# Kernel tuning notes

Hardware: AMD Instinct MI355X
Metric: run time of the kernel (lower is better)

The kernel has to match this reference:

```python
import jax, jax.numpy as jnp
import numpy as np

T, B = 256, 128
VOCAB, E, H, L = 73640, 320, 512, 5
G = 4 * H  # gate dim 2048


def setup_inputs() -> dict:
    key = jax.random.key(0)
    ks = jax.random.split(key, 12)
    stdv = 1.0 / np.sqrt(H)
    u = lambda k, shape: jax.random.uniform(k, shape, jnp.float32, -stdv, stdv)
    tokens = jax.random.randint(ks[0], (T, B), 0, VOCAB)
    embed = jax.random.normal(ks[1], (VOCAB, E), jnp.float32) * 0.1
    # layer 0 (input dim E), directions stacked on axis 0
    W_ih0 = u(ks[2], (2, G, E))
    W_hh0 = u(ks[3], (2, G, H))
    b_ih0 = u(ks[4], (2, G))
    b_hh0 = u(ks[5], (2, G))
    # layers 1..4 (input dim 2H = concat of both directions)
    W_ih = u(ks[6], (L - 1, 2, G, 2 * H))
    W_hh = u(ks[7], (L - 1, 2, G, H))
    b_ih = u(ks[8], (L - 1, 2, G))
    b_hh = u(ks[9], (L - 1, 2, G))
    return {"tokens": tokens, "embed": embed, "W_ih0": W_ih0, "W_hh0": W_hh0,
            "b_ih0": b_ih0, "b_hh0": b_hh0, "W_ih": W_ih, "W_hh": W_hh,
            "b_ih": b_ih, "b_hh": b_hh}


def _lstm_both_dirs(x, h, c, Wi, Wh, bi, bh):
    # x: [B, in]; h, c: [2, B, H]; Wi: [2, 4H, in]; Wh: [2, 4H, H]; bi, bh: [2, 4H]
    gates = (jnp.einsum('bi,dgi->dbg', x, Wi)
             + jnp.einsum('dbh,dgh->dbg', h, Wh)
             + (bi + bh)[:, None, :])
    i, f, g, o = jnp.split(gates, 4, axis=-1)  # PyTorch gate order i,f,g,o
    c_new = jax.nn.sigmoid(f) * c + jax.nn.sigmoid(i) * jnp.tanh(g)
    h_new = jax.nn.sigmoid(o) * jnp.tanh(c_new)
    return h_new, c_new


def reference(tokens, embed, W_ih0, W_hh0, b_ih0, b_hh0, W_ih, W_hh, b_ih, b_hh):
    emb = embed[tokens]  # [T, B, E]
    Bsz = tokens.shape[1]
    h0 = jnp.zeros((L, 2, Bsz, H), jnp.float32)
    c0 = jnp.zeros((L, 2, Bsz, H), jnp.float32)

    def step(carry, x_t):
        h, c = carry
        hl, cl = _lstm_both_dirs(x_t, h[0], c[0], W_ih0, W_hh0, b_ih0, b_hh0)
        hs, cs = [hl], [cl]
        inp = jnp.concatenate([hl[0], hl[1]], axis=-1)  # [B, 2H]
        for l in range(L - 1):
            hl, cl = _lstm_both_dirs(inp, h[l + 1], c[l + 1],
                                     W_ih[l], W_hh[l], b_ih[l], b_hh[l])
            hs.append(hl); cs.append(cl)
            inp = jnp.concatenate([hl[0], hl[1]], axis=-1)
        return (jnp.stack(hs), jnp.stack(cs)), hs[-1]  # emit last-layer h [2, B, H]

    _, last_layer_h = jax.lax.scan(step, (h0, c0), emb)  # [T, 2, B, H]
    # LASEREmbedderI: take last layer, max-pool over the two directions
    return jnp.max(last_layer_h, axis=1)  # [T, B, H]
```

## Files before the change

kernel.cpp:

```cpp
#include <hip/hip_runtime.h>
#include <stdint.h>

typedef unsigned short u16;
typedef unsigned int   u32;
typedef unsigned long long u64;
typedef short bf16x8 __attribute__((ext_vector_type(8)));
typedef float f32x4  __attribute__((ext_vector_type(4)));

static_assert(sizeof(bf16x8) == 16, "bf16x8 must be 16B");

#define LOG2E 1.4426950408889634f
#define TCH 32
#define NSLOT 131072
#define HDIR  65536

__device__ __forceinline__ float bf2f(u16 u) { return __builtin_bit_cast(float, ((u32)u) << 16); }
__device__ __forceinline__ u16 f2bf(float f) {
  u32 x = __builtin_bit_cast(u32, f);
  return (u16)((x + 0x7fffu + ((x >> 16) & 1u)) >> 16);
}
__device__ __forceinline__ float sigm(float x) {
  return __builtin_amdgcn_rcpf(1.f + __builtin_amdgcn_exp2f(-LOG2E * x));
}
__device__ __forceinline__ float tanh_(float x) {
  return 1.f - 2.f * __builtin_amdgcn_rcpf(1.f + __builtin_amdgcn_exp2f(2.f * LOG2E * x));
}
__device__ __forceinline__ bf16x8 cvt8(const float* p) {
  bf16x8 r;
  #pragma unroll
  for (int j = 0; j < 8; ++j) r[j] = (short)f2bf(p[j]);
  return r;
}

__global__ void k_bias(const float* __restrict__ bi0, const float* __restrict__ bh0,
                       const float* __restrict__ bi, const float* __restrict__ bh,
                       float* __restrict__ out) {
  int i = blockIdx.x * blockDim.x + threadIdx.x;
  if (i < 4096) out[i] = bi0[i] + bh0[i];
  else if (i < 20480) out[i] = bi[i - 4096] + bh[i - 4096];
}

__device__ __forceinline__ void gemm_tile(
    u16* smem, const u16* hb, const float* emb, const int* tok,
    const float* Wif, const float* bias, u16* gx, int K, int t0,
    int d, int nt0, int tt)
{
  u16* As = smem;
  u16* Bs = smem + 8192;
  int* s_tok = (int*)(smem + 16384);
  int tid = threadIdx.x, lane = tid & 63, w = tid >> 6;
  int wm = w & 1, wn = w >> 1;
  int t = t0 + tt;
  if (tok && tid < 128) s_tok[tid] = tok[t * 128 + tid];
  __syncthreads();

  const float* Bbase = Wif + ((size_t)d * 2048 + nt0 * 128) * K;
  f32x4 acc[4][4];
  #pragma unroll
  for (int a = 0; a < 4; ++a)
    #pragma unroll
    for (int b = 0; b < 4; ++b) acc[a][b] = f32x4{0.f, 0.f, 0.f, 0.f};

  int nkt = K >> 6;
  for (int kt = 0; kt < nkt; ++kt) {
    #pragma unroll
    for (int i = 0; i < 4; ++i) {
      int s = tid + i * 256;
      int row = s >> 3, c = s & 7;
      int cs = c ^ (row & 7);
      bf16x8 va;
      if (tok) {
        va = cvt8(emb + (size_t)s_tok[row] * 320 + kt * 64 + c * 8);
      } else {
        int k = kt * 64 + c * 8;
        va = *(const bf16x8*)(hb + (size_t)(t + 1) * NSLOT + (size_t)(k >> 9) * HDIR
                              + (size_t)row * 512 + (k & 511));
      }
      bf16x8 vb = cvt8(Bbase + (size_t)row * K + kt * 64 + c * 8);
      *(bf16x8*)(&As[(row * 8 + cs) * 8]) = va;
      *(bf16x8*)(&Bs[(row * 8 + cs) * 8]) = vb;
    }
    __syncthreads();
    #pragma unroll
    for (int kk2 = 0; kk2 < 2; ++kk2) {
      int cl = kk2 * 4 + (lane >> 4);
      bf16x8 af[4], bfr[4];
      #pragma unroll
      for (int mt = 0; mt < 4; ++mt) {
        int row = wm * 64 + mt * 16 + (lane & 15);
        af[mt] = *(const bf16x8*)(&As[(row * 8 + (cl ^ (row & 7))) * 8]);
      }
      #pragma unroll
      for (int nt = 0; nt < 4; ++nt) {
        int row = wn * 64 + nt * 16 + (lane & 15);
        bfr[nt] = *(const bf16x8*)(&Bs[(row * 8 + (cl ^ (row & 7))) * 8]);
      }
      #pragma unroll
      for (int mt = 0; mt < 4; ++mt)
        #pragma unroll
        for (int nt = 0; nt < 4; ++nt)
          acc[mt][nt] = __builtin_amdgcn_mfma_f32_16x16x32_bf16(af[mt], bfr[nt], acc[mt][nt], 0, 0, 0);
    }
    __syncthreads();
  }
  #pragma unroll
  for (int nt = 0; nt < 4; ++nt) {
    int g = nt0 * 128 + wn * 64 + nt * 16 + (lane & 15);
    float bv = bias[d * 2048 + g];
    int q = g >> 9, hbb = (g >> 4) & 31, u = g & 15;
    size_t cb = (((size_t)d * 32 + hbb) * TCH + tt) * 8192;
    #pragma unroll
    for (int mt = 0; mt < 4; ++mt)
      #pragma unroll
      for (int r = 0; r < 4; ++r) {
        int b = wm * 64 + mt * 16 + (lane >> 4) * 4 + r;
        int ws2 = b >> 5, mts = (b >> 4) & 1, l4s = (b >> 2) & 3, rs = b & 3;
        gx[cb + (size_t)(ws2 * 64 + l4s * 16 + u) * 32 + mts * 16 + q * 4 + rs]
          = f2bf(acc[mt][nt][r] + bv);
      }
  }
}

__global__ __launch_bounds__(256) void k_gemm0(
    const float* __restrict__ emb, const int* __restrict__ tok,
    const float* __restrict__ Wif, const float* __restrict__ bias, u16* __restrict__ gx)
{
  __shared__ __align__(16) u16 smem[16640];
  int xt = blockIdx.x;
  gemm_tile(smem, nullptr, emb, tok, Wif, bias, gx, 320, 0, xt >> 4, xt & 15, blockIdx.y);
}

__device__ __forceinline__ void waitflags(const u32* fl, int lane, int w, u32 target) {
  const u32* p = fl + ((lane & 31) << 4) + w;
  u32 v;
  for (;;) {
    asm volatile("global_load_dword %0, %1, off sc0 sc1\n\ts_waitcnt vmcnt(0)"
                 : "=v"(v) : "v"(p) : "memory");
    if (__all((int)(v >= target))) break;
    __builtin_amdgcn_s_sleep(1);
  }
}

__global__ __launch_bounds__(256, 2) void k_fused(
    const float* __restrict__ Whf, const u16* __restrict__ gx_s,
    u16* __restrict__ hb, float* __restrict__ cbuf,
    u32* flags, u32 base, int t0, int hz,
    const float* __restrict__ emb, const int* __restrict__ tok_g,
    const float* __restrict__ Wif_g, const float* __restrict__ bias_g,
    u16* __restrict__ gx_g, int Kg, int t0g)
{
  __shared__ __align__(16) u16 smem[32768];
  int tid = threadIdx.x, lane = tid & 63, w = tid >> 6;

  if (blockIdx.x >= 64) {
    if (t0g < 0) return;
    #pragma unroll 1
    for (int i = 0; i < 4; ++i) {
      int tau = (blockIdx.x - 64) + i * 256;
      int xt = tau & 31, tt = tau >> 5;
      gemm_tile(smem, hb, emb, tok_g, Wif_g, bias_g, gx_g, Kg, t0g, xt >> 4, xt & 15, tt);
      __syncthreads();
    }
    return;
  }

  int d = blockIdx.x >> 5, hb_i = blockIdx.x & 31;
  const u32* fl = flags + d * 512;
  u32* myflag = flags + d * 512 + hb_i * 16 + w;
  u16* WhL = smem;
  for (int i = tid; i < 64 * 512; i += 256) {
    int r = i >> 9, k = i & 511;
    int grow = (r >> 4) * 512 + hb_i * 16 + (r & 15);
    WhL[(r << 9) + (k ^ ((r & 7) << 3))] = f2bf(Whf[((size_t)d * 2048 + grow) * 512 + k]);
  }

  int bb = w * 32;
  int l15 = lane & 15, l4 = lane >> 4;
  float c2[2][4];
  if (t0 == 0) {
    #pragma unroll
    for (int mt = 0; mt < 2; ++mt)
      #pragma unroll
      for (int r = 0; r < 4; ++r) c2[mt][r] = 0.f;
  } else {
    #pragma unroll
    for (int mt = 0; mt < 2; ++mt)
      #pragma unroll
      for (int r = 0; r < 4; ++r) {
        int b = bb + mt * 16 + l4 * 4 + r;
        c2[mt][r] = cbuf[((size_t)d * 128 + b) * 512 + hb_i * 16 + l15];
      }
  }
  if (hz) {
    for (int i = tid; i < 512; i += 256) {
      int b = i >> 2, j = i & 3;
      u64* p = (u64*)(hb + (size_t)d * HDIR + (size_t)b * 512 + hb_i * 16) + j;
      __hip_atomic_store(p, 0ull, __ATOMIC_RELAXED, __HIP_MEMORY_SCOPE_AGENT);
    }
  }
  __syncthreads();
  if (hz && lane == 0) {
    u32 iv = base + 1;
    asm volatile("global_store_dword %0, %1, off sc0 sc1" :: "v"(myflag), "v"(iv) : "memory");
  }
  int init1 = hz ? 1 : 0;
  __builtin_amdgcn_s_setprio(1);

  const u16* gxblk = gx_s + ((size_t)d * 32 + hb_i) * TCH * 8192 + (size_t)tid * 32;
  bf16x8 gxv4[4], gxn4[4];
  #pragma unroll
  for (int j = 0; j < 4; ++j) gxv4[j] = *(const bf16x8*)(gxblk + j * 8);
  #pragma unroll
  for (int j = 0; j < 4; ++j) gxn4[j] = *(const bf16x8*)(gxblk + 8192 + j * 8);

  for (int tt = 0; tt < TCH; ++tt) {
    int t = t0 + tt;
    u32 target = base + (u32)tt + (u32)init1;
    if (!(tt == 0 && !init1)) waitflags(fl, lane, w, target);

    const u16* hp = hb + (size_t)t * NSLOT + (size_t)d * HDIR;
    const u16* hpA = hp + (size_t)(bb + l15) * 512 + l4 * 8;
    const u16* hpB = hp + (size_t)(bb + 16 + l15) * 512 + l4 * 8;
    f32x4 h0[16], h1[16];
    asm volatile(
      "global_load_dwordx4 %0, %8, off sc0 sc1\n\t"
      "global_load_dwordx4 %1, %8, off offset:64 sc0 sc1\n\t"
      "global_load_dwordx4 %2, %8, off offset:128 sc0 sc1\n\t"
      "global_load_dwordx4 %3, %8, off offset:192 sc0 sc1\n\t"
      "global_load_dwordx4 %4, %8, off offset:256 sc0 sc1\n\t"
      "global_load_dwordx4 %5, %8, off offset:320 sc0 sc1\n\t"
      "global_load_dwordx4 %6, %8, off offset:384 sc0 sc1\n\t"
      "global_load_dwordx4 %7, %8, off offset:448 sc0 sc1"
      : "=&v"(h0[0]), "=&v"(h0[1]), "=&v"(h0[2]), "=&v"(h0[3]),
        "=&v"(h0[4]), "=&v"(h0[5]), "=&v"(h0[6]), "=&v"(h0[7])
      : "v"(hpA) : "memory");
    asm volatile(
      "global_load_dwordx4 %0, %8, off offset:512 sc0 sc1\n\t"
      "global_load_dwordx4 %1, %8, off offset:576 sc0 sc1\n\t"
      "global_load_dwordx4 %2, %8, off offset:640 sc0 sc1\n\t"
      "global_load_dwordx4 %3, %8, off offset:704 sc0 sc1\n\t"
      "global_load_dwordx4 %4, %8, off offset:768 sc0 sc1\n\t"
      "global_load_dwordx4 %5, %8, off offset:832 sc0 sc1\n\t"
      "global_load_dwordx4 %6, %8, off offset:896 sc0 sc1\n\t"
      "global_load_dwordx4 %7, %8, off offset:960 sc0 sc1"
      : "=&v"(h0[8]), "=&v"(h0[9]), "=&v"(h0[10]), "=&v"(h0[11]),
        "=&v"(h0[12]), "=&v"(h0[13]), "=&v"(h0[14]), "=&v"(h0[15])
      : "v"(hpA) : "memory");
    asm volatile(
      "global_load_dwordx4 %0, %8, off sc0 sc1\n\t"
      "global_load_dwordx4 %1, %8, off offset:64 sc0 sc1\n\t"
      "global_load_dwordx4 %2, %8, off offset:128 sc0 sc1\n\t"
      "global_load_dwordx4 %3, %8, off offset:192 sc0 sc1\n\t"
      "global_load_dwordx4 %4, %8, off offset:256 sc0 sc1\n\t"
      "global_load_dwordx4 %5, %8, off offset:320 sc0 sc1\n\t"
      "global_load_dwordx4 %6, %8, off offset:384 sc0 sc1\n\t"
      "global_load_dwordx4 %7, %8, off offset:448 sc0 sc1"
      : "=&v"(h1[0]), "=&v"(h1[1]), "=&v"(h1[2]), "=&v"(h1[3]),
        "=&v"(h1[4]), "=&v"(h1[5]), "=&v"(h1[6]), "=&v"(h1[7])
      : "v"(hpB) : "memory");
    asm volatile(
      "global_load_dwordx4 %0, %8, off offset:512 sc0 sc1\n\t"
      "global_load_dwordx4 %1, %8, off offset:576 sc0 sc1\n\t"
      "global_load_dwordx4 %2, %8, off offset:640 sc0 sc1\n\t"
      "global_load_dwordx4 %3, %8, off offset:704 sc0 sc1\n\t"
      "global_load_dwordx4 %4, %8, off offset:768 sc0 sc1\n\t"
      "global_load_dwordx4 %5, %8, off offset:832 sc0 sc1\n\t"
      "global_load_dwordx4 %6, %8, off offset:896 sc0 sc1\n\t"
      "global_load_dwordx4 %7, %8, off offset:960 sc0 sc1\n\t"
      "s_waitcnt vmcnt(0)"
      : "=&v"(h1[8]), "=&v"(h1[9]), "=&v"(h1[10]), "=&v"(h1[11]),
        "=&v"(h1[12]), "=&v"(h1[13]), "=&v"(h1[14]), "=&v"(h1[15])
      : "v"(hpB) : "memory");
    __builtin_amdgcn_sched_barrier(0);

    f32x4 acc[2][4];
    #pragma unroll
    for (int mt = 0; mt < 2; ++mt)
      #pragma unroll
      for (int q = 0; q < 4; ++q) acc[mt][q] = f32x4{0.f, 0.f, 0.f, 0.f};
    #pragma unroll
    for (int kk = 0; kk < 16; ++kk) {
      int kbase = kk * 32 + l4 * 8;
      bf16x8 a0 = __builtin_bit_cast(bf16x8, h0[kk]);
      bf16x8 a1 = __builtin_bit_cast(bf16x8, h1[kk]);
      #pragma unroll
      for (int q = 0; q < 4; ++q) {
        int r = q * 16 + l15;
        bf16x8 bv = *(const bf16x8*)(&WhL[(r << 9) + (kbase ^ ((r & 7) << 3))]);
        acc[0][q] = __builtin_amdgcn_mfma_f32_16x16x32_bf16(a0, bv, acc[0][q], 0, 0, 0);
        acc[1][q] = __builtin_amdgcn_mfma_f32_16x16x32_bf16(a1, bv, acc[1][q], 0, 0, 0);
      }
    }
    u16* ho = hb + (size_t)(t + 1) * NSLOT + (size_t)d * HDIR;
    u32 hvv[2][4];
    #pragma unroll
    for (int mt = 0; mt < 2; ++mt)
      #pragma unroll
      for (int r = 0; r < 4; ++r) {
        float gi = acc[mt][0][r] + bf2f((u16)gxv4[mt * 2][r]);
        float gf = acc[mt][1][r] + bf2f((u16)gxv4[mt * 2][4 + r]);
        float gg = acc[mt][2][r] + bf2f((u16)gxv4[mt * 2 + 1][r]);
        float go = acc[mt][3][r] + bf2f((u16)gxv4[mt * 2 + 1][4 + r]);
        float cn = sigm(gf) * c2[mt][r] + sigm(gi) * tanh_(gg);
        float hn = sigm(go) * tanh_(cn);
        c2[mt][r] = cn;
        hvv[mt][r] = (u32)f2bf(hn);
      }
    {
      u16* st0 = ho + (size_t)(bb + l4 * 4) * 512 + hb_i * 16 + l15;
      u16* st1 = st0 + 16 * 512;
      int tt2 = (tt + 2 < TCH) ? (tt + 2) : (TCH - 1);
      const u16* gaddr = gxblk + (size_t)tt2 * 8192;
      u32 fv = target + 1;
      f32x4 g0, g1, g2, g3;
      asm volatile(
        "global_store_short %13, %4, off sc0 sc1\n\t"
        "global_store_short %13, %5, off offset:1024 sc0 sc1\n\t"
        "global_store_short %13, %6, off offset:2048 sc0 sc1\n\t"
        "global_store_short %13, %7, off offset:3072 sc0 sc1\n\t"
        "global_store_short %14, %8, off sc0 sc1\n\t"
        "global_store_short %14, %9, off offset:1024 sc0 sc1\n\t"
        "global_store_short %14, %10, off offset:2048 sc0 sc1\n\t"
        "global_store_short %14, %11, off offset:3072 sc0 sc1\n\t"
        "global_load_dwordx4 %0, %15, off\n\t"
        "global_load_dwordx4 %1, %15, off offset:16\n\t"
        "global_load_dwordx4 %2, %15, off offset:32\n\t"
        "global_load_dwordx4 %3, %15, off offset:48\n\t"
        "s_waitcnt vmcnt(4)\n\t"
        "global_store_dword %16, %12, off sc0 sc1"
        : "=&v"(g0), "=&v"(g1), "=&v"(g2), "=&v"(g3)
        : "v"(hvv[0][0]), "v"(hvv[0][1]), "v"(hvv[0][2]), "v"(hvv[0][3]),
          "v"(hvv[1][0]), "v"(hvv[1][1]), "v"(hvv[1][2]), "v"(hvv[1][3]),
          "v"(fv), "v"(st0), "v"(st1), "v"(gaddr), "v"(myflag)
        : "memory");
      #pragma unroll
      for (int j = 0; j < 4; ++j) gxv4[j] = gxn4[j];
      gxn4[0] = __builtin_bit_cast(bf16x8, g0);
      gxn4[1] = __builtin_bit_cast(bf16x8, g1);
      gxn4[2] = __builtin_bit_cast(bf16x8, g2);
      gxn4[3] = __builtin_bit_cast(bf16x8, g3);
    }
  }
  #pragma unroll
  for (int mt = 0; mt < 2; ++mt)
    #pragma unroll
    for (int r = 0; r < 4; ++r) {
      int b = bb + mt * 16 + l4 * 4 + r;
      cbuf[((size_t)d * 128 + b) * 512 + hb_i * 16 + l15] = c2[mt][r];
    }
}

__global__ void k_final(const u16* __restrict__ hb, float* __restrict__ out, int n) {
  int i = blockIdx.x * 256 + threadIdx.x;
  if (i >= n) return;
  int t = i >> 16, rem = i & 65535;
  int b = rem >> 9, j = rem & 511;
  const u16* s = hb + (size_t)(t + 1) * NSLOT + (size_t)b * 512 + j;
  float a = bf2f(s[0]);
  float bv = bf2f(s[HDIR]);
  out[i] = fmaxf(a, bv);
}

extern "C" void kernel_launch(void* const* d_in, const int* in_sizes, int n_in,
                              void* d_out, int out_size, void* d_ws, size_t ws_size,
                              hipStream_t stream) {
  (void)in_sizes; (void)n_in; (void)out_size; (void)ws_size;
  const int*   tokens = (const int*)d_in[0];
  const float* embedW = (const float*)d_in[1];
  const float* W_ih0  = (const float*)d_in[2];
  const float* W_hh0  = (const float*)d_in[3];
  const float* b_ih0  = (const float*)d_in[4];
  const float* b_hh0  = (const float*)d_in[5];
  const float* W_ih   = (const float*)d_in[6];
  const float* W_hh   = (const float*)d_in[7];
  const float* b_ih   = (const float*)d_in[8];
  const float* b_hh   = (const float*)d_in[9];

  char* ws = (char*)d_ws;
  size_t off = 0;
  auto alloc = [&](size_t bytes) { void* p = ws + off; off += (bytes + 255) & ~(size_t)255; return p; };
  float* biasC = (float*)alloc(20480ull * 4);
  u16*   hbuf  = (u16*)alloc((size_t)257 * NSLOT * 2);
  u16*   gxA   = (u16*)alloc(16777216ull * 2);
  u16*   gxB   = (u16*)alloc(16777216ull * 2);
  float* cbuf  = (float*)alloc(131072ull * 4);
  u32*   flags = (u32*)alloc(8192);

  hipMemsetAsync(flags, 0, 8192, stream);
  k_bias<<<80, 256, 0, stream>>>(b_ih0, b_hh0, b_ih, b_hh, biasC);
  k_gemm0<<<dim3(32, 32), 256, 0, stream>>>(embedW, tokens, W_ih0, biasC, gxA);

  u32 base = 0;
  for (int l = 0; l < 5; ++l) {
    const float* Whf_l = l ? (W_hh + (size_t)(l - 1) * 2097152) : W_hh0;
    for (int c = 0; c < 8; ++c) {
      int g = l * 8 + c;
      u16* gx_s = (g & 1) ? gxB : gxA;
      u16* gx_g = (g & 1) ? gxA : gxB;
      int lg = (c < 7) ? l : l + 1;
      int cg = (c < 7) ? c + 1 : 0;
      int has_g = (lg <= 4);
      const float* Wif_g = (lg == 0) ? W_ih0 : (W_ih + (size_t)(lg - 1) * 4194304);
      const int* tok_g = (lg == 0) ? tokens : nullptr;
      int Kg = (lg == 0) ? 320 : 1024;
      k_fused<<<320, 256, 0, stream>>>(
          Whf_l, gx_s, hbuf, cbuf, flags, base, c * TCH, (l == 0 && c == 0) ? 1 : 0,
          embedW, tok_g, Wif_g, biasC + (size_t)lg * 4096, gx_g, Kg,
          has_g ? cg * TCH : -1);
      base += 40;
    }
  }
  k_final<<<65536, 256, 0, stream>>>(hbuf, (float*)d_out, 16777216);
}
```

Measured before the change: 10.25 ms.

## Run LSTM layers as a diagonal wavefront over time chunks

Replaces the layer-by-layer sequence of 40 fused launches with 36 wavefront launches. Each launch runs the recurrent scan for every (layer, chunk) cell on the current anti-diagonal, plus the input-projection GEMMs for the next diagonal, and the chunk size drops from 32 to 8 steps. GEMM tiles wait on flags from the layer below rather than on launch order. Hidden-state storage becomes a 16-slot ring per layer. The final direction max-pool moves into the last layer through atomicMax on order-preserving encoded floats, followed by a decode pass. The goal is to overlap the serial recurrence of different layers and use more CUs at once, at the cost of more cross-block spin-waiting, atomics on the output, and shorter chunks with more per-launch setup.

```diff
diff --git a/kernel.cpp b/kernel.cpp
--- a/kernel.cpp
+++ b/kernel.cpp
@@ -10,9 +10,10 @@
 static_assert(sizeof(bf16x8) == 16, "bf16x8 must be 16B");
 
 #define LOG2E 1.4426950408889634f
-#define TCH 32
+#define TCH 8
 #define NSLOT 131072
 #define HDIR  65536
+#define GXCELL 4194304ull
 
 __device__ __forceinline__ float bf2f(u16 u) { return __builtin_bit_cast(float, ((u32)u) << 16); }
 __device__ __forceinline__ u16 f2bf(float f) {
@@ -30,6 +31,10 @@
   #pragma unroll
   for (int j = 0; j < 8; ++j) r[j] = (short)f2bf(p[j]);
   return r;
+}
+__device__ __forceinline__ u32 encf(float f) {
+  u32 b = __builtin_bit_cast(u32, f);
+  return (b & 0x80000000u) ? ~b : (b | 0x80000000u);
 }
 
 __global__ void k_bias(const float* __restrict__ bi0, const float* __restrict__ bh0,
@@ -41,20 +46,21 @@
 }
 
 __device__ __forceinline__ void gemm_tile(
-    u16* smem, const u16* hb, const float* emb, const int* tok,
-    const float* Wif, const float* bias, u16* gx, int K, int t0,
-    int d, int nt0, int tt)
+    u16* smem, const u16* hbPrev, const float* emb, const int* tok,
+    const float* Wif, const float* bias, u16* gx, int K,
+    int c, int tt, int d, int nt0)
 {
   u16* As = smem;
   u16* Bs = smem + 8192;
   int* s_tok = (int*)(smem + 16384);
   int tid = threadIdx.x, lane = tid & 63, w = tid >> 6;
   int wm = w & 1, wn = w >> 1;
-  int t = t0 + tt;
+  int t = c * TCH + tt;
   if (tok && tid < 128) s_tok[tid] = tok[t * 128 + tid];
   __syncthreads();
 
   const float* Bbase = Wif + ((size_t)d * 2048 + nt0 * 128) * K;
+  int slot = (t + 1) & 15;
   f32x4 acc[4][4];
   #pragma unroll
   for (int a = 0; a < 4; ++a)
@@ -66,17 +72,17 @@
     #pragma unroll
     for (int i = 0; i < 4; ++i) {
       int s = tid + i * 256;
-      int row = s >> 3, c = s & 7;
-      int cs = c ^ (row & 7);
+      int row = s >> 3, cc = s & 7;
+      int cs = cc ^ (row & 7);
       bf16x8 va;
       if (tok) {
-        va = cvt8(emb + (size_t)s_tok[row] * 320 + kt * 64 + c * 8);
+        va = cvt8(emb + (size_t)s_tok[row] * 320 + kt * 64 + cc * 8);
       } else {
-        int k = kt * 64 + c * 8;
-        va = *(const bf16x8*)(hb + (size_t)(t + 1) * NSLOT + (size_t)(k >> 9) * HDIR
+        int k = kt * 64 + cc * 8;
+        va = *(const bf16x8*)(hbPrev + (size_t)slot * NSLOT + (size_t)(k >> 9) * HDIR
                               + (size_t)row * 512 + (k & 511));
       }
-      bf16x8 vb = cvt8(Bbase + (size_t)row * K + kt * 64 + c * 8);
+      bf16x8 vb = cvt8(Bbase + (size_t)row * K + kt * 64 + cc * 8);
       *(bf16x8*)(&As[(row * 8 + cs) * 8]) = va;
       *(bf16x8*)(&Bs[(row * 8 + cs) * 8]) = vb;
     }
@@ -127,46 +133,137 @@
 {
   __shared__ __align__(16) u16 smem[16640];
   int xt = blockIdx.x;
-  gemm_tile(smem, nullptr, emb, tok, Wif, bias, gx, 320, 0, xt >> 4, xt & 15, blockIdx.y);
+  gemm_tile(smem, nullptr, emb, tok, Wif, bias, gx, 320, 0, blockIdx.y, xt >> 4, xt & 15);
 }
 
 __device__ __forceinline__ void waitflags(const u32* fl, int lane, int w, u32 target) {
   const u32* p = fl + ((lane & 31) << 4) + w;
-  u32 v;
   for (;;) {
+    u32 v;
     asm volatile("global_load_dword %0, %1, off sc0 sc1\n\ts_waitcnt vmcnt(0)"
                  : "=v"(v) : "v"(p) : "memory");
     if (__all((int)(v >= target))) break;
     __builtin_amdgcn_s_sleep(1);
   }
 }
-
-__global__ __launch_bounds__(256, 2) void k_fused(
-    const float* __restrict__ Whf, const u16* __restrict__ gx_s,
-    u16* __restrict__ hb, float* __restrict__ cbuf,
-    u32* flags, u32 base, int t0, int hz,
-    const float* __restrict__ emb, const int* __restrict__ tok_g,
-    const float* __restrict__ Wif_g, const float* __restrict__ bias_g,
-    u16* __restrict__ gx_g, int Kg, int t0g)
+__device__ __forceinline__ void wait_all(const u32* flp, int lane, u32 target) {
+  const u32* p = flp + lane * 16;
+  for (;;) {
+    f32x4 v4;
+    asm volatile("global_load_dwordx4 %0, %1, off sc0 sc1\n\ts_waitcnt vmcnt(0)"
+                 : "=v"(v4) : "v"(p) : "memory");
+    u32 m0 = __builtin_bit_cast(u32, v4[0]), m1 = __builtin_bit_cast(u32, v4[1]);
+    u32 m2 = __builtin_bit_cast(u32, v4[2]), m3 = __builtin_bit_cast(u32, v4[3]);
+    u32 mn = m0 < m1 ? m0 : m1; mn = mn < m2 ? mn : m2; mn = mn < m3 ? mn : m3;
+    if (__all((int)(mn >= target))) break;
+    __builtin_amdgcn_s_sleep(2);
+  }
+}
+
+#define HB8A(P, D) \
+    asm volatile( \
+      "global_load_dwordx4 %0, %8, off sc0 sc1\n\t" \
+      "global_load_dwordx4 %1, %8, off offset:64 sc0 sc1\n\t" \
+      "global_load_dwordx4 %2, %8, off offset:128 sc0 sc1\n\t" \
+      "global_load_dwordx4 %3, %8, off offset:192 sc0 sc1\n\t" \
+      "global_load_dwordx4 %4, %8, off offset:256 sc0 sc1\n\t" \
+      "global_load_dwordx4 %5, %8, off offset:320 sc0 sc1\n\t" \
+      "global_load_dwordx4 %6, %8, off offset:384 sc0 sc1\n\t" \
+      "global_load_dwordx4 %7, %8, off offset:448 sc0 sc1" \
+      : "=&v"(D[0]), "=&v"(D[1]), "=&v"(D[2]), "=&v"(D[3]), \
+        "=&v"(D[4]), "=&v"(D[5]), "=&v"(D[6]), "=&v"(D[7]) \
+      : "v"(P) : "memory")
+#define HB8B(P, D) \
+    asm volatile( \
+      "global_load_dwordx4 %0, %8, off offset:512 sc0 sc1\n\t" \
+      "global_load_dwordx4 %1, %8, off offset:576 sc0 sc1\n\t" \
+      "global_load_dwordx4 %2, %8, off offset:640 sc0 sc1\n\t" \
+      "global_load_dwordx4 %3, %8, off offset:704 sc0 sc1\n\t" \
+      "global_load_dwordx4 %4, %8, off offset:768 sc0 sc1\n\t" \
+      "global_load_dwordx4 %5, %8, off offset:832 sc0 sc1\n\t" \
+      "global_load_dwordx4 %6, %8, off offset:896 sc0 sc1\n\t" \
+      "global_load_dwordx4 %7, %8, off offset:960 sc0 sc1" \
+      : "=&v"(D[8]), "=&v"(D[9]), "=&v"(D[10]), "=&v"(D[11]), \
+        "=&v"(D[12]), "=&v"(D[13]), "=&v"(D[14]), "=&v"(D[15]) \
+      : "v"(P) : "memory")
+
+#define STPF_BODY(FLAGOPS) \
+      asm volatile( \
+        "global_store_short %13, %4, off sc0 sc1\n\t" \
+        "global_store_short %13, %5, off offset:1024 sc0 sc1\n\t" \
+        "global_store_short %13, %6, off offset:2048 sc0 sc1\n\t" \
+        "global_store_short %13, %7, off offset:3072 sc0 sc1\n\t" \
+        "global_store_short %14, %8, off sc0 sc1\n\t" \
+        "global_store_short %14, %9, off offset:1024 sc0 sc1\n\t" \
+        "global_store_short %14, %10, off offset:2048 sc0 sc1\n\t" \
+        "global_store_short %14, %11, off offset:3072 sc0 sc1\n\t" \
+        "global_load_dwordx4 %0, %15, off\n\t" \
+        "global_load_dwordx4 %1, %15, off offset:16\n\t" \
+        "global_load_dwordx4 %2, %15, off offset:32\n\t" \
+        "global_load_dwordx4 %3, %15, off offset:48\n\t" \
+        "s_waitcnt vmcnt(4)\n\t" \
+        FLAGOPS \
+        : "=&v"(g0), "=&v"(g1), "=&v"(g2), "=&v"(g3) \
+        : "v"(hvv[0][0]), "v"(hvv[0][1]), "v"(hvv[0][2]), "v"(hvv[0][3]), \
+          "v"(hvv[1][0]), "v"(hvv[1][1]), "v"(hvv[1][2]), "v"(hvv[1][3]), \
+          "v"(fv), "v"(st0), "v"(st1), "v"(gaddr), "v"(myflag) \
+        : "memory")
+
+__global__ __launch_bounds__(256, 2) void k_wave(
+    int g,
+    const float* __restrict__ W_hh0, const float* __restrict__ W_hh,
+    const float* __restrict__ W_ih0, const float* __restrict__ W_ih,
+    const float* __restrict__ biasC, const float* __restrict__ emb,
+    const int* __restrict__ tok,
+    u16* __restrict__ hbuf, u16* __restrict__ gxb, float* __restrict__ cbuf,
+    u32* __restrict__ outU, u32* __restrict__ flags)
 {
   __shared__ __align__(16) u16 smem[32768];
   int tid = threadIdx.x, lane = tid & 63, w = tid >> 6;
-
-  if (blockIdx.x >= 64) {
-    if (t0g < 0) return;
+  int bx = blockIdx.x;
+  int llo_s = (g - 31 > 0) ? (g - 31) : 0;
+  int lhi_s = (g < 4) ? g : 4;
+  int nscan = lhi_s - llo_s + 1;
+
+  if (bx >= 64 * nscan) {
+    int D = g + 1;
+    if (D > 35) return;
+    int llo = (D - 31 > 0) ? (D - 31) : 0;
+    int lhi = (D < 4) ? D : 4;
+    int ncell = lhi - llo + 1;
+    int J = ncell * 256;
+    int gid = bx - 64 * nscan, NG = 512 - 64 * nscan;
     #pragma unroll 1
-    for (int i = 0; i < 4; ++i) {
-      int tau = (blockIdx.x - 64) + i * 256;
-      int xt = tau & 31, tt = tau >> 5;
-      gemm_tile(smem, hb, emb, tok_g, Wif_g, bias_g, gx_g, Kg, t0g, xt >> 4, xt & 15, tt);
+    for (int j = gid; j < J; j += NG) {
+      int tt = j / (ncell * 32);
+      int rem = j - tt * (ncell * 32);
+      int ci = rem >> 5, dnt = rem & 31;
+      int lg = llo + ci, cg = D - lg;
+      const float* Wif = lg ? (W_ih + (size_t)(lg - 1) * 4194304) : W_ih0;
+      int K = lg ? 1024 : 320;
+      const int* tokp = lg ? nullptr : tok;
+      const u16* hbPrev = lg ? (hbuf + (size_t)(lg - 1) * 16 * NSLOT) : nullptr;
+      u16* gxd = gxb + ((size_t)(lg * 2 + (cg & 1))) * GXCELL;
+      if (lg > 0 && w == 0)
+        wait_all(flags + (size_t)(lg - 1) * 1024, lane, 40u * cg + 2u + (u32)tt);
+      gemm_tile(smem, hbPrev, emb, tokp, Wif, biasC + (size_t)lg * 4096,
+                gxd, K, cg, tt, dnt >> 4, dnt & 15);
       __syncthreads();
     }
     return;
   }
 
-  int d = blockIdx.x >> 5, hb_i = blockIdx.x & 31;
-  const u32* fl = flags + d * 512;
-  u32* myflag = flags + d * 512 + hb_i * 16 + w;
+  int ci = bx >> 6, within = bx & 63;
+  int l = llo_s + ci, c = g - l;
+  int d = within >> 5, hb_i = within & 31;
+  const float* Whf = l ? (W_hh + (size_t)(l - 1) * 2097152) : W_hh0;
+  u16* hbL = hbuf + (size_t)l * 16 * NSLOT;
+  float* cbL = cbuf + (size_t)l * 131072;
+  const u16* gxs = gxb + ((size_t)(l * 2 + (c & 1))) * GXCELL;
+  u32* fl = flags + (size_t)l * 1024 + d * 512;
+  u32* myflag = fl + hb_i * 16 + w;
+  u32 base = 40u * (u32)c;
+
   u16* WhL = smem;
   for (int i = tid; i < 64 * 512; i += 256) {
     int r = i >> 9, k = i & 511;
@@ -177,100 +274,53 @@
   int bb = w * 32;
   int l15 = lane & 15, l4 = lane >> 4;
   float c2[2][4];
-  if (t0 == 0) {
+  if (c == 0) {
     #pragma unroll
     for (int mt = 0; mt < 2; ++mt)
       #pragma unroll
       for (int r = 0; r < 4; ++r) c2[mt][r] = 0.f;
+    for (int i = tid; i < 512; i += 256) {
+      int b = i >> 2, j = i & 3;
+      u64* p = (u64*)(hbL + (size_t)d * HDIR + (size_t)b * 512 + hb_i * 16) + j;
+      __hip_atomic_store(p, 0ull, __ATOMIC_RELAXED, __HIP_MEMORY_SCOPE_AGENT);
+    }
+    __syncthreads();
+    if (lane == 0) {
+      u32 iv = base + 1;
+      asm volatile("global_store_dword %0, %1, off sc0 sc1" :: "v"(myflag), "v"(iv) : "memory");
+    }
+    waitflags(fl, lane, w, base + 1);
   } else {
     #pragma unroll
     for (int mt = 0; mt < 2; ++mt)
       #pragma unroll
       for (int r = 0; r < 4; ++r) {
         int b = bb + mt * 16 + l4 * 4 + r;
-        c2[mt][r] = cbuf[((size_t)d * 128 + b) * 512 + hb_i * 16 + l15];
-      }
-  }
-  if (hz) {
-    for (int i = tid; i < 512; i += 256) {
-      int b = i >> 2, j = i & 3;
-      u64* p = (u64*)(hb + (size_t)d * HDIR + (size_t)b * 512 + hb_i * 16) + j;
-      __hip_atomic_store(p, 0ull, __ATOMIC_RELAXED, __HIP_MEMORY_SCOPE_AGENT);
-    }
-  }
-  __syncthreads();
-  if (hz && lane == 0) {
-    u32 iv = base + 1;
-    asm volatile("global_store_dword %0, %1, off sc0 sc1" :: "v"(myflag), "v"(iv) : "memory");
-  }
-  int init1 = hz ? 1 : 0;
+        c2[mt][r] = cbL[((size_t)d * 128 + b) * 512 + hb_i * 16 + l15];
+      }
+    __syncthreads();
+  }
   __builtin_amdgcn_s_setprio(1);
 
-  const u16* gxblk = gx_s + ((size_t)d * 32 + hb_i) * TCH * 8192 + (size_t)tid * 32;
+  const u16* gxblk = gxs + ((size_t)(d * 32 + hb_i) * TCH) * 8192 + (size_t)tid * 32;
   bf16x8 gxv4[4], gxn4[4];
   #pragma unroll
   for (int j = 0; j < 4; ++j) gxv4[j] = *(const bf16x8*)(gxblk + j * 8);
   #pragma unroll
   for (int j = 0; j < 4; ++j) gxn4[j] = *(const bf16x8*)(gxblk + 8192 + j * 8);
 
+  #pragma unroll 1
   for (int tt = 0; tt < TCH; ++tt) {
-    int t = t0 + tt;
-    u32 target = base + (u32)tt + (u32)init1;
-    if (!(tt == 0 && !init1)) waitflags(fl, lane, w, target);
-
-    const u16* hp = hb + (size_t)t * NSLOT + (size_t)d * HDIR;
+    int t = c * TCH + tt;
+    if (tt > 0) waitflags(fl, lane, w, base + 1 + (u32)tt);
+
+    const u16* hp = hbL + (size_t)(t & 15) * NSLOT + (size_t)d * HDIR;
     const u16* hpA = hp + (size_t)(bb + l15) * 512 + l4 * 8;
     const u16* hpB = hp + (size_t)(bb + 16 + l15) * 512 + l4 * 8;
     f32x4 h0[16], h1[16];
-    asm volatile(
-      "global_load_dwordx4 %0, %8, off sc0 sc1\n\t"
-      "global_load_dwordx4 %1, %8, off offset:64 sc0 sc1\n\t"
-      "global_load_dwordx4 %2, %8, off offset:128 sc0 sc1\n\t"
-      "global_load_dwordx4 %3, %8, off offset:192 sc0 sc1\n\t"
-      "global_load_dwordx4 %4, %8, off offset:256 sc0 sc1\n\t"
-      "global_load_dwordx4 %5, %8, off offset:320 sc0 sc1\n\t"
-      "global_load_dwordx4 %6, %8, off offset:384 sc0 sc1\n\t"
-      "global_load_dwordx4 %7, %8, off offset:448 sc0 sc1"
-      : "=&v"(h0[0]), "=&v"(h0[1]), "=&v"(h0[2]), "=&v"(h0[3]),
-        "=&v"(h0[4]), "=&v"(h0[5]), "=&v"(h0[6]), "=&v"(h0[7])
-      : "v"(hpA) : "memory");
-    asm volatile(
-      "global_load_dwordx4 %0, %8, off offset:512 sc0 sc1\n\t"
-      "global_load_dwordx4 %1, %8, off offset:576 sc0 sc1\n\t"
-      "global_load_dwordx4 %2, %8, off offset:640 sc0 sc1\n\t"
-      "global_load_dwordx4 %3, %8, off offset:704 sc0 sc1\n\t"
-      "global_load_dwordx4 %4, %8, off offset:768 sc0 sc1\n\t"
-      "global_load_dwordx4 %5, %8, off offset:832 sc0 sc1\n\t"
-      "global_load_dwordx4 %6, %8, off offset:896 sc0 sc1\n\t"
-      "global_load_dwordx4 %7, %8, off offset:960 sc0 sc1"
-      : "=&v"(h0[8]), "=&v"(h0[9]), "=&v"(h0[10]), "=&v"(h0[11]),
-        "=&v"(h0[12]), "=&v"(h0[13]), "=&v"(h0[14]), "=&v"(h0[15])
-      : "v"(hpA) : "memory");
-    asm volatile(
-      "global_load_dwordx4 %0, %8, off sc0 sc1\n\t"
-      "global_load_dwordx4 %1, %8, off offset:64 sc0 sc1\n\t"
-      "global_load_dwordx4 %2, %8, off offset:128 sc0 sc1\n\t"
-      "global_load_dwordx4 %3, %8, off offset:192 sc0 sc1\n\t"
-      "global_load_dwordx4 %4, %8, off offset:256 sc0 sc1\n\t"
-      "global_load_dwordx4 %5, %8, off offset:320 sc0 sc1\n\t"
-      "global_load_dwordx4 %6, %8, off offset:384 sc0 sc1\n\t"
-      "global_load_dwordx4 %7, %8, off offset:448 sc0 sc1"
-      : "=&v"(h1[0]), "=&v"(h1[1]), "=&v"(h1[2]), "=&v"(h1[3]),
-        "=&v"(h1[4]), "=&v"(h1[5]), "=&v"(h1[6]), "=&v"(h1[7])
-      : "v"(hpB) : "memory");
-    asm volatile(
-      "global_load_dwordx4 %0, %8, off offset:512 sc0 sc1\n\t"
-      "global_load_dwordx4 %1, %8, off offset:576 sc0 sc1\n\t"
-      "global_load_dwordx4 %2, %8, off offset:640 sc0 sc1\n\t"
-      "global_load_dwordx4 %3, %8, off offset:704 sc0 sc1\n\t"
-      "global_load_dwordx4 %4, %8, off offset:768 sc0 sc1\n\t"
-      "global_load_dwordx4 %5, %8, off offset:832 sc0 sc1\n\t"
-      "global_load_dwordx4 %6, %8, off offset:896 sc0 sc1\n\t"
-      "global_load_dwordx4 %7, %8, off offset:960 sc0 sc1\n\t"
-      "s_waitcnt vmcnt(0)"
-      : "=&v"(h1[8]), "=&v"(h1[9]), "=&v"(h1[10]), "=&v"(h1[11]),
-        "=&v"(h1[12]), "=&v"(h1[13]), "=&v"(h1[14]), "=&v"(h1[15])
-      : "v"(hpB) : "memory");
+    HB8A(hpA, h0); HB8B(hpA, h0);
+    HB8A(hpB, h1); HB8B(hpB, h1);
+    asm volatile("s_waitcnt vmcnt(0)" ::: "memory");
     __builtin_amdgcn_sched_barrier(0);
 
     f32x4 acc[2][4];
@@ -291,8 +341,9 @@
         acc[1][q] = __builtin_amdgcn_mfma_f32_16x16x32_bf16(a1, bv, acc[1][q], 0, 0, 0);
       }
     }
-    u16* ho = hb + (size_t)(t + 1) * NSLOT + (size_t)d * HDIR;
+    u16* ho = hbL + (size_t)((t + 1) & 15) * NSLOT + (size_t)d * HDIR;
     u32 hvv[2][4];
+    float hnf[2][4];
     #pragma unroll
     for (int mt = 0; mt < 2; ++mt)
       #pragma unroll
@@ -304,6 +355,7 @@
         float cn = sigm(gf) * c2[mt][r] + sigm(gi) * tanh_(gg);
         float hn = sigm(go) * tanh_(cn);
         c2[mt][r] = cn;
+        hnf[mt][r] = hn;
         hvv[mt][r] = (u32)f2bf(hn);
       }
     {
@@ -311,28 +363,19 @@
       u16* st1 = st0 + 16 * 512;
       int tt2 = (tt + 2 < TCH) ? (tt + 2) : (TCH - 1);
       const u16* gaddr = gxblk + (size_t)tt2 * 8192;
-      u32 fv = target + 1;
+      u32 fv = base + 2 + (u32)tt;
       f32x4 g0, g1, g2, g3;
-      asm volatile(
-        "global_store_short %13, %4, off sc0 sc1\n\t"
-        "global_store_short %13, %5, off offset:1024 sc0 sc1\n\t"
-        "global_store_short %13, %6, off offset:2048 sc0 sc1\n\t"
-        "global_store_short %13, %7, off offset:3072 sc0 sc1\n\t"
-        "global_store_short %14, %8, off sc0 sc1\n\t"
-        "global_store_short %14, %9, off offset:1024 sc0 sc1\n\t"
-        "global_store_short %14, %10, off offset:2048 sc0 sc1\n\t"
-        "global_store_short %14, %11, off offset:3072 sc0 sc1\n\t"
-        "global_load_dwordx4 %0, %15, off\n\t"
-        "global_load_dwordx4 %1, %15, off offset:16\n\t"
-        "global_load_dwordx4 %2, %15, off offset:32\n\t"
-        "global_load_dwordx4 %3, %15, off offset:48\n\t"
-        "s_waitcnt vmcnt(4)\n\t"
-        "global_store_dword %16, %12, off sc0 sc1"
-        : "=&v"(g0), "=&v"(g1), "=&v"(g2), "=&v"(g3)
-        : "v"(hvv[0][0]), "v"(hvv[0][1]), "v"(hvv[0][2]), "v"(hvv[0][3]),
-          "v"(hvv[1][0]), "v"(hvv[1][1]), "v"(hvv[1][2]), "v"(hvv[1][3]),
-          "v"(fv), "v"(st0), "v"(st1), "v"(gaddr), "v"(myflag)
-        : "memory");
+      if (lane == 0) { STPF_BODY("global_store_dword %16, %12, off sc0 sc1"); }
+      else          { STPF_BODY("s_nop 0"); }
+      if (l == 4) {
+        #pragma unroll
+        for (int mt = 0; mt < 2; ++mt)
+          #pragma unroll
+          for (int r = 0; r < 4; ++r) {
+            int b = bb + mt * 16 + l4 * 4 + r;
+            atomicMax(&outU[((size_t)t * 128 + b) * 512 + hb_i * 16 + l15], encf(hnf[mt][r]));
+          }
+      }
       #pragma unroll
       for (int j = 0; j < 4; ++j) gxv4[j] = gxn4[j];
       gxn4[0] = __builtin_bit_cast(bf16x8, g0);
@@ -346,19 +389,16 @@
     #pragma unroll
     for (int r = 0; r < 4; ++r) {
       int b = bb + mt * 16 + l4 * 4 + r;
-      cbuf[((size_t)d * 128 + b) * 512 + hb_i * 16 + l15] = c2[mt][r];
-    }
-}
-
-__global__ void k_final(const u16* __restrict__ hb, float* __restrict__ out, int n) {
+      cbL[((size_t)d * 128 + b) * 512 + hb_i * 16 + l15] = c2[mt][r];
+    }
+}
+
+__global__ void k_decode(u32* __restrict__ p, int n) {
   int i = blockIdx.x * 256 + threadIdx.x;
   if (i >= n) return;
-  int t = i >> 16, rem = i & 65535;
-  int b = rem >> 9, j = rem & 511;
-  const u16* s = hb + (size_t)(t + 1) * NSLOT + (size_t)b * 512 + j;
-  float a = bf2f(s[0]);
-  float bv = bf2f(s[HDIR]);
-  out[i] = fmaxf(a, bv);
+  u32 u = p[i];
+  u32 b = (u & 0x80000000u) ? (u ^ 0x80000000u) : ~u;
+  p[i] = b;
 }
 
 extern "C" void kernel_launch(void* const* d_in, const int* in_sizes, int n_in,
@@ -380,35 +420,20 @@
   size_t off = 0;
   auto alloc = [&](size_t bytes) { void* p = ws + off; off += (bytes + 255) & ~(size_t)255; return p; };
   float* biasC = (float*)alloc(20480ull * 4);
-  u16*   hbuf  = (u16*)alloc((size_t)257 * NSLOT * 2);
-  u16*   gxA   = (u16*)alloc(16777216ull * 2);
-  u16*   gxB   = (u16*)alloc(16777216ull * 2);
-  float* cbuf  = (float*)alloc(131072ull * 4);
-  u32*   flags = (u32*)alloc(8192);
-
-  hipMemsetAsync(flags, 0, 8192, stream);
+  u16*   hbuf  = (u16*)alloc((size_t)5 * 16 * NSLOT * 2);
+  u16*   gxb   = (u16*)alloc((size_t)10 * GXCELL * 2);
+  float* cbuf  = (float*)alloc((size_t)5 * 131072 * 4);
+  u32*   flags = (u32*)alloc(32768);
+
+  hipMemsetAsync(flags, 0, 32768, stream);
+  hipMemsetAsync(d_out, 0, (size_t)16777216 * 4, stream);
   k_bias<<<80, 256, 0, stream>>>(b_ih0, b_hh0, b_ih, b_hh, biasC);
-  k_gemm0<<<dim3(32, 32), 256, 0, stream>>>(embedW, tokens, W_ih0, biasC, gxA);
-
-  u32 base = 0;
-  for (int l = 0; l < 5; ++l) {
-    const float* Whf_l = l ? (W_hh + (size_t)(l - 1) * 2097152) : W_hh0;
-    for (int c = 0; c < 8; ++c) {
-      int g = l * 8 + c;
-      u16* gx_s = (g & 1) ? gxB : gxA;
-      u16* gx_g = (g & 1) ? gxA : gxB;
-      int lg = (c < 7) ? l : l + 1;
-      int cg = (c < 7) ? c + 1 : 0;
-      int has_g = (lg <= 4);
-      const float* Wif_g = (lg == 0) ? W_ih0 : (W_ih + (size_t)(lg - 1) * 4194304);
-      const int* tok_g = (lg == 0) ? tokens : nullptr;
-      int Kg = (lg == 0) ? 320 : 1024;
-      k_fused<<<320, 256, 0, stream>>>(
-          Whf_l, gx_s, hbuf, cbuf, flags, base, c * TCH, (l == 0 && c == 0) ? 1 : 0,
-          embedW, tok_g, Wif_g, biasC + (size_t)lg * 4096, gx_g, Kg,
-          has_g ? cg * TCH : -1);
-      base += 40;
-    }
-  }
-  k_final<<<65536, 256, 0, stream>>>(hbuf, (float*)d_out, 16777216);
-}
+  k_gemm0<<<dim3(32, TCH), 256, 0, stream>>>(embedW, tokens, W_ih0, biasC, gxb);
+
+  for (int g = 0; g < 36; ++g) {
+    k_wave<<<512, 256, 0, stream>>>(g, W_hh0, W_hh, W_ih0, W_ih, biasC,
+                                    embedW, tokens, hbuf, gxb, cbuf,
+                                    (u32*)d_out, flags);
+  }
+  k_decode<<<65536, 256, 0, stream>>>((u32*)d_out, 16777216);
+}
```

New measurement: 9.650 ms. 1.06x faster.
